# Optimization experiments

Hardware: AMD Instinct MI355X
Metric: run time of the kernel (lower is better)

The kernel has to match this reference:

```python
import jax, jax.numpy as jnp
import numpy as np

N = 100000       # num nodes
E = 1600000      # num edges
IN_DIM = 128
HID = 128
HEADS = 4
HEAD_DIM = HID // HEADS  # 32
NEG_SLOPE = 0.2
LN_EPS = 1e-5


def _glorot(key, shape):
    fan_in, fan_out = shape[-1], shape[0]
    limit = float(np.sqrt(6.0 / (fan_in + fan_out)))
    return jax.random.uniform(key, shape, jnp.float32, -limit, limit)


def setup_inputs() -> dict:
    key = jax.random.key(0)
    ks = jax.random.split(key, 16)
    return {
        "x": jax.random.normal(ks[0], (N, IN_DIM), jnp.float32),
        "edge_index": jax.random.randint(ks[1], (2, E), 0, N, jnp.int64),
        # embedding Linear(IN_DIM -> HID)
        "W_emb": _glorot(ks[2], (HID, IN_DIM)),
        "b_emb": jnp.zeros((HID,), jnp.float32),
        # E8 layer weight (F.linear, no bias)
        "W_e8": _glorot(ks[3], (HID, HID)),
        # GATConv: lin weight [HID, HEADS*HEAD_DIM], attention vectors, output bias
        "W_gat": _glorot(ks[4], (HEADS * HEAD_DIM, HID)),
        "att_src": _glorot(ks[5], (HEADS, HEAD_DIM)),
        "att_dst": _glorot(ks[6], (HEADS, HEAD_DIM)),
        "b_gat": jnp.zeros((HEADS * HEAD_DIM,), jnp.float32),
        # fusion Linear(2*HID -> HID)
        "W_fus": _glorot(ks[7], (HID, 2 * HID)),
        "b_fus": jnp.zeros((HID,), jnp.float32),
        # LayerNorm(HID)
        "gamma": jnp.ones((HID,), jnp.float32),
        "beta": jnp.zeros((HID,), jnp.float32),
        # readout MLP HID -> HID//2 -> 1
        "W_r1": _glorot(ks[8], (HID // 2, HID)),
        "b_r1": jnp.zeros((HID // 2,), jnp.float32),
        "W_r2": _glorot(ks[9], (1, HID // 2)),
        "b_r2": jnp.zeros((1,), jnp.float32),
    }


def reference(x, edge_index, W_emb, b_emb, W_e8, W_gat, att_src, att_dst,
              b_gat, W_fus, b_fus, gamma, beta, W_r1, b_r1, W_r2, b_r2):
    row = edge_index[0]  # src
    col = edge_index[1]  # dst

    # embedding
    h = x @ W_emb.T + b_emb          # [N, HID]
    res = h

    # --- E8: sparse normalized-adjacency matmul + linear ---
    deg = jax.ops.segment_sum(jnp.ones((E,), h.dtype), col, num_segments=N)
    dinv = jnp.where(deg > 0, deg ** -0.5, 0.0)
    vals = dinv[row] * dinv[col]                       # [E]
    agg = jax.ops.segment_sum(h[col] * vals[:, None], row, num_segments=N)
    x_e8 = agg @ W_e8.T                                # [N, HID]

    # --- GATConv (heads=4, concat, add_self_loops) ---
    loop = jnp.arange(N, dtype=row.dtype)
    src = jnp.concatenate([row, loop])                 # [E+N]
    dst = jnp.concatenate([col, loop])
    g = (h @ W_gat.T).reshape(N, HEADS, HEAD_DIM)      # [N, H, C]
    a_src = (g * att_src).sum(-1)                      # [N, H]
    a_dst = (g * att_dst).sum(-1)
    e = jax.nn.leaky_relu(a_src[src] + a_dst[dst], NEG_SLOPE)  # [E+N, H]
    m = jax.ops.segment_max(e, dst, num_segments=N)    # scatter-softmax max
    e = jnp.exp(e - m[dst])
    s = jax.ops.segment_sum(e, dst, num_segments=N)
    alpha = e / (s[dst] + 1e-16)                       # [E+N, H]
    msg = g[src] * alpha[..., None]                    # [E+N, H, C]
    x_gat = jax.ops.segment_sum(msg, dst, num_segments=N).reshape(N, HEADS * HEAD_DIM) + b_gat

    # --- fusion + residual + LayerNorm + ReLU ---
    f = jnp.concatenate([x_e8, x_gat], axis=-1) @ W_fus.T + b_fus
    z = f + res
    mu = z.mean(-1, keepdims=True)
    var = ((z - mu) ** 2).mean(-1, keepdims=True)
    z = (z - mu) * jax.lax.rsqrt(var + LN_EPS) * gamma + beta
    z = jax.nn.relu(z)  # dropout is identity in eval mode

    # --- readout MLP + sigmoid ---
    r = jax.nn.relu(z @ W_r1.T + b_r1)
    out = jax.nn.sigmoid(r @ W_r2.T + b_r2)            # [N, 1]
    return out
```

## Files before the change

kernel.cpp:

```cpp
#include <hip/hip_runtime.h>
#include <hip/hip_bf16.h>
#include <math.h>

#define NWIN 16
#define NCHUNK 128
#define CAP 64

typedef __attribute__((ext_vector_type(8))) short bf16x8;
typedef __attribute__((ext_vector_type(4))) float f32x4;
typedef __attribute__((ext_vector_type(2))) int i32x2;

__device__ __forceinline__ float us2f(unsigned short u) {
    return __uint_as_float(((unsigned)u) << 16);
}
__device__ __forceinline__ unsigned short f2bf(float f) {
    unsigned u = __float_as_uint(f);
    u += 0x7FFF + ((u >> 16) & 1);
    return (unsigned short)(u >> 16);
}

__global__ void setup_kernel(const float* __restrict__ b_gat, const float* __restrict__ W_fus,
                             const float* __restrict__ b_fus, float* __restrict__ bfus2,
                             const float* __restrict__ We, const float* __restrict__ W8,
                             const float* __restrict__ Wg, unsigned short* __restrict__ W16,
                             int* __restrict__ cnt, int total) {
    int b = blockIdx.x;
    if (b == 0) {
        int t = threadIdx.x;
        if (t < 128) {
            float acc = b_fus[t];
            for (int k = 0; k < 128; k++)
                acc += b_gat[k] * W_fus[t * 256 + 128 + k];
            bfus2[t] = acc;
        }
        return;
    }
    if (b <= 320) {
        int i = (b - 1) * 256 + threadIdx.x;
        if (i < 81920) {
            float v;
            if (i < 16384) v = We[i];
            else if (i < 32768) v = W8[i - 16384];
            else if (i < 49152) v = Wg[i - 32768];
            else v = W_fus[i - 49152];
            W16[i] = f2bf(v);
        }
        return;
    }
    int i = (b - 321) * 256 + threadIdx.x;
    if (i < total) cnt[i] = 0;
}

__global__ __launch_bounds__(256) void fill_win(
    const int* __restrict__ row, const int* __restrict__ col,
    int* __restrict__ cnt, int* __restrict__ adjF, int E, int N, int win) {
    int b = blockIdx.x;
    int w = (b & 7) | (((b >> 10) & 1) << 3);
    int chunk = (b >> 3) & (NCHUNK - 1);
    int lo = w * win, hi = lo + win;
    int per = (E + NCHUNK - 1) / NCHUNK;
    per = (per + 1) & ~1;
    int s = chunk * per;
    int e_end = s + per; if (e_end > E) e_end = E;

    for (int i = s + threadIdx.x * 2; i < e_end; i += 512) {
        int r0, r1, c0, c1;
        if (i + 1 < e_end) {
            i32x2 rv = __builtin_nontemporal_load((const i32x2*)(row + i));
            i32x2 cv = __builtin_nontemporal_load((const i32x2*)(col + i));
            r0 = rv[0]; r1 = rv[1]; c0 = cv[0]; c1 = cv[1];
        } else {
            r0 = row[i]; r1 = -1;
            c0 = col[i]; c1 = 0;
        }
        if (c0 >= lo && c0 < hi) {
            int p = atomicAdd(&cnt[c0], 1);
            if (p < CAP) adjF[(size_t)c0 * CAP + p] = r0;
        }
        int k2 = N + r0;
        if (k2 >= lo && k2 < hi) {
            int p = atomicAdd(&cnt[k2], 1);
            if (p < CAP) adjF[(size_t)k2 * CAP + p] = c0;
        }
        if (r1 >= 0) {
            if (c1 >= lo && c1 < hi) {
                int p = atomicAdd(&cnt[c1], 1);
                if (p < CAP) adjF[(size_t)c1 * CAP + p] = r1;
            }
            int k3 = N + r1;
            if (k3 >= lo && k3 < hi) {
                int p = atomicAdd(&cnt[k3], 1);
                if (p < CAP) adjF[(size_t)k3 * CAP + p] = c1;
            }
        }
    }
}

__global__ void dinv_kernel(const int* __restrict__ cnt, float* __restrict__ dinv, int N) {
    int i = blockIdx.x * 256 + threadIdx.x;
    if (i < N) {
        int d = cnt[i];
        dinv[i] = d > 0 ? rsqrtf((float)d) : 0.0f;
    }
}

template <bool A_FP32, bool HAS_BIAS, bool OUT_BF16, bool OUT_SC, bool OUT_ATT>
__global__ __launch_bounds__(256) void gemm_mfma(
    const void* __restrict__ A_, const unsigned short* __restrict__ W16,
    const float* __restrict__ bias, unsigned short* __restrict__ C16,
    const float* __restrict__ rsc, unsigned short* __restrict__ Csc,
    const float* __restrict__ attS, const float* __restrict__ attD,
    float* __restrict__ aS, float* __restrict__ aD, int n) {
    const int t = threadIdx.x;
    const int wave = t >> 6, lane = t & 63;
    const int quad = lane >> 4, ln = lane & 15;
    const int row0 = blockIdx.x * 128 + wave * 32;
    const int kq = quad * 8;

    f32x4 zero = {0.f, 0.f, 0.f, 0.f};
    f32x4 acc[2][8];
#pragma unroll
    for (int i = 0; i < 2; i++)
#pragma unroll
        for (int j = 0; j < 8; j++) acc[i][j] = zero;

#pragma unroll
    for (int ks = 0; ks < 4; ks++) {
        bf16x8 a[2];
#pragma unroll
        for (int mt = 0; mt < 2; mt++) {
            int row = row0 + mt * 16 + ln;
            if (row >= n) row = n - 1;
            if (A_FP32) {
                const float* ap = (const float*)A_ + (size_t)row * 128 + ks * 32 + kq;
                float4 f0 = *(const float4*)ap;
                float4 f1 = *(const float4*)(ap + 4);
                bf16x8 v;
                v[0] = (short)f2bf(f0.x); v[1] = (short)f2bf(f0.y);
                v[2] = (short)f2bf(f0.z); v[3] = (short)f2bf(f0.w);
                v[4] = (short)f2bf(f1.x); v[5] = (short)f2bf(f1.y);
                v[6] = (short)f2bf(f1.z); v[7] = (short)f2bf(f1.w);
                a[mt] = v;
            } else {
                a[mt] = *(const bf16x8*)((const unsigned short*)A_ +
                                         (size_t)row * 128 + ks * 32 + kq);
            }
        }
#pragma unroll
        for (int nt = 0; nt < 8; nt++) {
            bf16x8 b = *(const bf16x8*)(W16 + (size_t)(nt * 16 + ln) * 128 + ks * 32 + kq);
            acc[0][nt] = __builtin_amdgcn_mfma_f32_16x16x32_bf16(a[0], b, acc[0][nt], 0, 0, 0);
            acc[1][nt] = __builtin_amdgcn_mfma_f32_16x16x32_bf16(a[1], b, acc[1][nt], 0, 0, 0);
        }
    }

    float bv[8];
    if (HAS_BIAS) {
#pragma unroll
        for (int nt = 0; nt < 8; nt++) bv[nt] = bias[nt * 16 + ln];
    }
    float asv[8], adv[8];
    if (OUT_ATT) {
#pragma unroll
        for (int nt = 0; nt < 8; nt++) {
            int idx = (nt >> 1) * 32 + (nt & 1) * 16 + ln;
            asv[nt] = attS[idx];
            adv[nt] = attD[idx];
        }
    }
#pragma unroll
    for (int mt = 0; mt < 2; mt++) {
        int rbase = row0 + mt * 16 + quad * 4;
#pragma unroll
        for (int reg = 0; reg < 4; reg++) {
            int row = rbase + reg;
            if (row >= n) continue;
            float sc = OUT_SC ? rsc[row] : 0.f;
            if (OUT_ATT) {
                float ps[4] = {0.f, 0.f, 0.f, 0.f};
                float pd[4] = {0.f, 0.f, 0.f, 0.f};
#pragma unroll
                for (int nt = 0; nt < 8; nt++) {
                    float v = acc[mt][nt][reg];
                    ps[nt >> 1] += v * asv[nt];
                    pd[nt >> 1] += v * adv[nt];
                }
#pragma unroll
                for (int m = 1; m < 16; m <<= 1) {
#pragma unroll
                    for (int hh = 0; hh < 4; hh++) {
                        ps[hh] += __shfl_xor(ps[hh], m);
                        pd[hh] += __shfl_xor(pd[hh], m);
                    }
                }
                if (ln == 0) {
                    *(float4*)&aS[(size_t)row * 4] = make_float4(ps[0], ps[1], ps[2], ps[3]);
                    *(float4*)&aD[(size_t)row * 4] = make_float4(pd[0], pd[1], pd[2], pd[3]);
                }
            }
#pragma unroll
            for (int nt = 0; nt < 8; nt++) {
                float v = acc[mt][nt][reg];
                if (HAS_BIAS) v += bv[nt];
                int col = nt * 16 + ln;
                if (OUT_BF16) C16[(size_t)row * 128 + col] = f2bf(v);
                if (OUT_SC) Csc[(size_t)row * 128 + col] = f2bf(v * sc);
            }
        }
    }
}

__global__ __launch_bounds__(256) void fusion_ln_mfma(
    const unsigned short* __restrict__ xe816, const unsigned short* __restrict__ xg16,
    const unsigned short* __restrict__ Wf16,
    const float* __restrict__ bfus2, const unsigned short* __restrict__ h16,
    const float* __restrict__ gamma, const float* __restrict__ beta,
    unsigned short* __restrict__ z16, int n) {
    const int t = threadIdx.x;
    const int wave = t >> 6, lane = t & 63;
    const int quad = lane >> 4, ln = lane & 15;
    const int row0 = blockIdx.x * 128 + wave * 32;
    const int kq = quad * 8;

    f32x4 zero = {0.f, 0.f, 0.f, 0.f};
    f32x4 acc[2][8];
#pragma unroll
    for (int i = 0; i < 2; i++)
#pragma unroll
        for (int j = 0; j < 8; j++) acc[i][j] = zero;

    for (int half = 0; half < 2; half++) {
        const unsigned short* A = half ? xg16 : xe816;
#pragma unroll
        for (int ks = 0; ks < 4; ks++) {
            bf16x8 a[2];
#pragma unroll
            for (int mt = 0; mt < 2; mt++) {
                int row = row0 + mt * 16 + ln;
                if (row >= n) row = n - 1;
                a[mt] = *(const bf16x8*)(A + (size_t)row * 128 + ks * 32 + kq);
            }
#pragma unroll
            for (int nt = 0; nt < 8; nt++) {
                bf16x8 b = *(const bf16x8*)(Wf16 + (size_t)(nt * 16 + ln) * 256 +
                                            half * 128 + ks * 32 + kq);
                acc[0][nt] = __builtin_amdgcn_mfma_f32_16x16x32_bf16(a[0], b, acc[0][nt], 0, 0, 0);
                acc[1][nt] = __builtin_amdgcn_mfma_f32_16x16x32_bf16(a[1], b, acc[1][nt], 0, 0, 0);
            }
        }
    }

    float bv[8], gm[8], bt[8];
#pragma unroll
    for (int nt = 0; nt < 8; nt++) {
        int c = nt * 16 + ln;
        bv[nt] = bfus2[c]; gm[nt] = gamma[c]; bt[nt] = beta[c];
    }
#pragma unroll
    for (int mt = 0; mt < 2; mt++) {
#pragma unroll
        for (int reg = 0; reg < 4; reg++) {
            int row = row0 + mt * 16 + quad * 4 + reg;
            if (row >= n) continue;
            float v[8];
            float s1 = 0.f, s2 = 0.f;
#pragma unroll
            for (int nt = 0; nt < 8; nt++) {
                float x = acc[mt][nt][reg] + bv[nt] +
                          us2f(h16[(size_t)row * 128 + nt * 16 + ln]);
                v[nt] = x; s1 += x; s2 += x * x;
            }
#pragma unroll
            for (int m = 1; m < 16; m <<= 1) {
                s1 += __shfl_xor(s1, m);
                s2 += __shfl_xor(s2, m);
            }
            float mu = s1 * (1.f / 128.f);
            float var = s2 * (1.f / 128.f) - mu * mu;
            float inv = rsqrtf(var + 1e-5f);
#pragma unroll
            for (int nt = 0; nt < 8; nt++) {
                float o = (v[nt] - mu) * inv * gm[nt] + bt[nt];
                o = o > 0.f ? o : 0.f;
                z16[(size_t)row * 128 + nt * 16 + ln] = f2bf(o);
            }
        }
    }
}

__global__ __launch_bounds__(256) void e8_gather(
    const int* __restrict__ cnt, const int* __restrict__ adjF,
    const float* __restrict__ dinv, const unsigned short* __restrict__ hd16,
    unsigned short* __restrict__ agg16, int N) {
    int r = blockIdx.x * 4 + (threadIdx.x >> 6);
    int lane = threadIdx.x & 63;
    if (r >= N) return;
    int key = N + r;
    int m = min(cnt[key], CAP);
    int av = (lane < m) ? adjF[(size_t)key * CAP + lane] : 0;
    float ax = 0.f, ay = 0.f;
    int j = 0;
    for (; j + 8 <= m; j += 8) {
        int c[8]; ushort2 hv[8];
#pragma unroll
        for (int q = 0; q < 8; q++) c[q] = __shfl(av, j + q);
#pragma unroll
        for (int q = 0; q < 8; q++)
            hv[q] = *(const ushort2*)&hd16[(size_t)c[q] * 128 + lane * 2];
#pragma unroll
        for (int q = 0; q < 8; q++) { ax += us2f(hv[q].x); ay += us2f(hv[q].y); }
    }
    for (; j < m; j++) {
        int c = __shfl(av, j);
        ushort2 hv = *(const ushort2*)&hd16[(size_t)c * 128 + lane * 2];
        ax += us2f(hv.x);
        ay += us2f(hv.y);
    }
    float dr = dinv[r];
    ushort2 o; o.x = f2bf(ax * dr); o.y = f2bf(ay * dr);
    *(ushort2*)&agg16[(size_t)r * 128 + lane * 2] = o;
}

__global__ __launch_bounds__(256) void gat_gather(
    const int* __restrict__ cnt, const int* __restrict__ adjF,
    const float* __restrict__ a_src, const float* __restrict__ a_dst,
    const unsigned short* __restrict__ g16, unsigned short* __restrict__ xg16, int N) {
    int d = blockIdx.x * 4 + (threadIdx.x >> 6);
    int lane = threadIdx.x & 63;
    if (d >= N) return;
    int hd = lane >> 4;
    float ad = a_dst[d * 4 + hd];

    float e = a_src[d * 4 + hd] + ad; e = e > 0.f ? e : 0.2f * e;
    float m0 = e, l = 1.f;
    ushort2 gv0 = *(const ushort2*)&g16[(size_t)d * 128 + lane * 2];
    float accx = us2f(gv0.x), accy = us2f(gv0.y);

    int mm = min(cnt[d], CAP);
    int av = (lane < mm) ? adjF[(size_t)d * CAP + lane] : 0;
    int j = 0;
    for (; j + 4 <= mm; j += 4) {
        int s[4]; float tv[4]; ushort2 gu[4];
#pragma unroll
        for (int q = 0; q < 4; q++) s[q] = __shfl(av, j + q);
#pragma unroll
        for (int q = 0; q < 4; q++) tv[q] = a_src[s[q] * 4 + hd];
#pragma unroll
        for (int q = 0; q < 4; q++)
            gu[q] = *(const ushort2*)&g16[(size_t)s[q] * 128 + lane * 2];
        float mn = m0;
#pragma unroll
        for (int q = 0; q < 4; q++) {
            tv[q] += ad;
            tv[q] = tv[q] > 0.f ? tv[q] : 0.2f * tv[q];
            mn = fmaxf(mn, tv[q]);
        }
        float sc = __expf(m0 - mn);
        float wsum = 0.f, axp = 0.f, ayp = 0.f;
#pragma unroll
        for (int q = 0; q < 4; q++) {
            float wq = __expf(tv[q] - mn);
            wsum += wq;
            axp += wq * us2f(gu[q].x);
            ayp += wq * us2f(gu[q].y);
        }
        accx = accx * sc + axp;
        accy = accy * sc + ayp;
        l = l * sc + wsum;
        m0 = mn;
    }
    for (; j < mm; j++) {
        int s = __shfl(av, j);
        float t0 = a_src[s * 4 + hd] + ad; t0 = t0 > 0.f ? t0 : 0.2f * t0;
        ushort2 gu = *(const ushort2*)&g16[(size_t)s * 128 + lane * 2];
        float mn = fmaxf(m0, t0);
        float sc = __expf(m0 - mn), w = __expf(t0 - mn);
        accx = accx * sc + w * us2f(gu.x);
        accy = accy * sc + w * us2f(gu.y);
        l = l * sc + w;
        m0 = mn;
    }
    float inv = 1.f / l;
    ushort2 o; o.x = f2bf(accx * inv); o.y = f2bf(accy * inv);
    *(ushort2*)&xg16[(size_t)d * 128 + lane * 2] = o;
}

__global__ __launch_bounds__(256) void readout_kernel(
    const unsigned short* __restrict__ z16, const float* __restrict__ W1,
    const float* __restrict__ b1, const float* __restrict__ W2,
    const float* __restrict__ b2, float* __restrict__ out, int N) {
    __shared__ float zs[32 * 132];
    __shared__ float wlds[64 * 132];
    __shared__ float w2s[64];
    __shared__ float b1s[64];
    const int t = threadIdx.x;
    const int row0 = blockIdx.x * 32;

    for (int i = 0; i < 4; i++) {
        int idx = i * 256 + t;
        int r = idx >> 5, c4 = idx & 31;
        float4 v = make_float4(0.f, 0.f, 0.f, 0.f);
        if (row0 + r < N) {
            ushort4 u = *(const ushort4*)&z16[(size_t)(row0 + r) * 128 + c4 * 4];
            v = make_float4(us2f(u.x), us2f(u.y), us2f(u.z), us2f(u.w));
        }
        *(float4*)&zs[r * 132 + c4 * 4] = v;
    }
    for (int i = 0; i < 8; i++) {
        int idx = i * 256 + t;
        int o = idx >> 5, c4 = idx & 31;
        *(float4*)&wlds[o * 132 + c4 * 4] = *(const float4*)&W1[o * 128 + c4 * 4];
    }
    if (t < 64) { w2s[t] = W2[t]; b1s[t] = b1[t]; }
    __syncthreads();

    const int rg = t >> 4;
    const int cg = t & 15;
    float acc[2][4] = {};
    const float* z0 = &zs[(rg * 2) * 132];
    const float* z1 = z0 + 132;
    for (int k4 = 0; k4 < 32; k4++) {
        float4 a0 = *(const float4*)&z0[k4 * 4];
        float4 a1 = *(const float4*)&z1[k4 * 4];
#pragma unroll
        for (int j = 0; j < 4; j++) {
            float4 wv = *(const float4*)&wlds[(cg * 4 + j) * 132 + k4 * 4];
            acc[0][j] += a0.x * wv.x + a0.y * wv.y + a0.z * wv.z + a0.w * wv.w;
            acc[1][j] += a1.x * wv.x + a1.y * wv.y + a1.z * wv.z + a1.w * wv.w;
        }
    }
    float p0 = 0.f, p1 = 0.f;
#pragma unroll
    for (int j = 0; j < 4; j++) {
        int o = cg * 4 + j;
        float r0 = acc[0][j] + b1s[o]; r0 = r0 > 0.f ? r0 : 0.f;
        float r1 = acc[1][j] + b1s[o]; r1 = r1 > 0.f ? r1 : 0.f;
        p0 += r0 * w2s[o]; p1 += r1 * w2s[o];
    }
    for (int off = 8; off > 0; off >>= 1) {
        p0 += __shfl_down(p0, off, 16);
        p1 += __shfl_down(p1, off, 16);
    }
    if (cg == 0) {
        float bb = b2[0];
        int r0i = row0 + rg * 2, r1i = r0i + 1;
        if (r0i < N) out[r0i] = 1.f / (1.f + __expf(-(p0 + bb)));
        if (r1i < N) out[r1i] = 1.f / (1.f + __expf(-(p1 + bb)));
    }
}

extern "C" void kernel_launch(void* const* d_in, const int* in_sizes, int n_in,
                              void* d_out, int out_size, void* d_ws, size_t ws_size,
                              hipStream_t stream) {
    const float* x     = (const float*)d_in[0];
    const int*   ei    = (const int*)d_in[1];
    const float* W_emb = (const float*)d_in[2];
    const float* b_emb = (const float*)d_in[3];
    const float* W_e8  = (const float*)d_in[4];
    const float* W_gat = (const float*)d_in[5];
    const float* att_s = (const float*)d_in[6];
    const float* att_d = (const float*)d_in[7];
    const float* b_gat = (const float*)d_in[8];
    const float* W_fus = (const float*)d_in[9];
    const float* b_fus = (const float*)d_in[10];
    const float* gamma = (const float*)d_in[11];
    const float* beta  = (const float*)d_in[12];
    const float* W_r1  = (const float*)d_in[13];
    const float* b_r1  = (const float*)d_in[14];
    const float* W_r2  = (const float*)d_in[15];
    const float* b_r2  = (const float*)d_in[16];

    const int N = in_sizes[0] / 128;
    const int E = in_sizes[1] / 2;
    const int* rowp = ei;
    const int* colp = ei + E;
    const int total = 2 * N;
    const int win = (total + NWIN - 1) / NWIN;
    const int GB = (N + 127) / 128;

    const size_t NF = (size_t)N * 128;
    char* base = (char*)d_ws;
    unsigned short* h16   = (unsigned short*)base;
    unsigned short* hd16  = h16 + NF;
    unsigned short* bufA  = hd16 + NF;
    unsigned short* xe816 = bufA + NF;
    unsigned short* g16   = xe816 + NF;
    int*            adjF  = (int*)(g16 + NF);
    unsigned short* z16   = (unsigned short*)adjF;
    float* dinv  = (float*)(adjF + NF);
    float* a_src = dinv + N;
    float* a_dst = a_src + (size_t)4 * N;
    float* bfus2 = a_dst + (size_t)4 * N;
    unsigned short* W16a = (unsigned short*)(bfus2 + 128);
    unsigned short* We16 = W16a;
    unsigned short* W816 = W16a + 16384;
    unsigned short* Wg16 = W16a + 32768;
    unsigned short* Wf16 = W16a + 49152;
    int* cnt = (int*)(W16a + 81920);

    int setup_grid = 321 + (total + 255) / 256;
    setup_kernel<<<setup_grid, 256, 0, stream>>>(b_gat, W_fus, b_fus, bfus2,
                                                 W_emb, W_e8, W_gat, W16a, cnt, total);
    fill_win<<<2048, 256, 0, stream>>>(rowp, colp, cnt, adjF, E, N, win);
    dinv_kernel<<<(N + 255) / 256, 256, 0, stream>>>(cnt, dinv, N);

    gemm_mfma<true, true, true, true, false><<<GB, 256, 0, stream>>>(
        x, We16, b_emb, h16, dinv, hd16, nullptr, nullptr, nullptr, nullptr, N);

    e8_gather<<<(N + 3) / 4, 256, 0, stream>>>(cnt, adjF, dinv, hd16, bufA, N);
    gemm_mfma<false, false, true, false, false><<<GB, 256, 0, stream>>>(
        bufA, W816, nullptr, xe816, nullptr, nullptr, nullptr, nullptr,
        nullptr, nullptr, N);

    gemm_mfma<false, false, true, false, true><<<GB, 256, 0, stream>>>(
        h16, Wg16, nullptr, g16, nullptr, nullptr, att_s, att_d, a_src, a_dst, N);
    gat_gather<<<(N + 3) / 4, 256, 0, stream>>>(cnt, adjF, a_src, a_dst, g16, bufA, N);

    fusion_ln_mfma<<<GB, 256, 0, stream>>>(xe816, bufA, Wf16, bfus2, h16,
                                           gamma, beta, z16, N);

    readout_kernel<<<(N + 31) / 32, 256, 0, stream>>>(z16, W_r1, b_r1, W_r2, b_r2,
                                                      (float*)d_out, N);
}
```

Baseline: 625.8 us.

## Co-schedule independent GEMM and gather stages in combined kernel launches

Independent stages now share a launch by splitting the grid on block index. The embedding GEMM runs alongside the adjacency fill, the GAT projection GEMM alongside the E8 gather, and the E8 weight GEMM alongside the GAT softmax gather. This cuts the launch count and lets compute-bound GEMM blocks overlap with memory-bound gather blocks. Other changes: E8 now reads dinv per neighbor instead of a prescaled copy of h, the GAT softmax computes the max in one wave-wide pass instead of an online rescale, and the fill window/chunk counts and nontemporal loads are changed. Costs include an extra dinv read per edge and register pressure from mixing kernel bodies in one launch.

Measured after the change: 789.2 us. 1.26x slower.

```diff
diff --git a/kernel.cpp b/kernel.cpp
--- a/kernel.cpp
+++ b/kernel.cpp
@@ -2,13 +2,12 @@
 #include <hip/hip_bf16.h>
 #include <math.h>
 
-#define NWIN 16
-#define NCHUNK 128
+#define NWIN 8
+#define NCHUNK 256
 #define CAP 64
 
 typedef __attribute__((ext_vector_type(8))) short bf16x8;
 typedef __attribute__((ext_vector_type(4))) float f32x4;
-typedef __attribute__((ext_vector_type(2))) int i32x2;
 
 __device__ __forceinline__ float us2f(unsigned short u) {
     return __uint_as_float(((unsigned)u) << 16);
@@ -51,70 +50,59 @@
     if (i < total) cnt[i] = 0;
 }
 
-__global__ __launch_bounds__(256) void fill_win(
-    const int* __restrict__ row, const int* __restrict__ col,
+__device__ __forceinline__ void fill_body(
+    int bid, const int* __restrict__ row, const int* __restrict__ col,
     int* __restrict__ cnt, int* __restrict__ adjF, int E, int N, int win) {
-    int b = blockIdx.x;
-    int w = (b & 7) | (((b >> 10) & 1) << 3);
-    int chunk = (b >> 3) & (NCHUNK - 1);
+    int w = bid & (NWIN - 1);
+    int chunk = bid >> 3;
     int lo = w * win, hi = lo + win;
     int per = (E + NCHUNK - 1) / NCHUNK;
     per = (per + 1) & ~1;
     int s = chunk * per;
     int e_end = s + per; if (e_end > E) e_end = E;
 
-    for (int i = s + threadIdx.x * 2; i < e_end; i += 512) {
-        int r0, r1, c0, c1;
+    for (int i = s + (int)threadIdx.x * 2; i < e_end; i += 512) {
+        int2 rv, cv;
         if (i + 1 < e_end) {
-            i32x2 rv = __builtin_nontemporal_load((const i32x2*)(row + i));
-            i32x2 cv = __builtin_nontemporal_load((const i32x2*)(col + i));
-            r0 = rv[0]; r1 = rv[1]; c0 = cv[0]; c1 = cv[1];
+            rv = *(const int2*)(row + i);
+            cv = *(const int2*)(col + i);
         } else {
-            r0 = row[i]; r1 = -1;
-            c0 = col[i]; c1 = 0;
-        }
-        if (c0 >= lo && c0 < hi) {
-            int p = atomicAdd(&cnt[c0], 1);
-            if (p < CAP) adjF[(size_t)c0 * CAP + p] = r0;
-        }
-        int k2 = N + r0;
+            rv.x = row[i]; rv.y = -1;
+            cv.x = col[i]; cv.y = 0;
+        }
+        if (cv.x >= lo && cv.x < hi) {
+            int p = atomicAdd(&cnt[cv.x], 1);
+            if (p < CAP) adjF[(size_t)cv.x * CAP + p] = rv.x;
+        }
+        int k2 = N + rv.x;
         if (k2 >= lo && k2 < hi) {
             int p = atomicAdd(&cnt[k2], 1);
-            if (p < CAP) adjF[(size_t)k2 * CAP + p] = c0;
-        }
-        if (r1 >= 0) {
-            if (c1 >= lo && c1 < hi) {
-                int p = atomicAdd(&cnt[c1], 1);
-                if (p < CAP) adjF[(size_t)c1 * CAP + p] = r1;
-            }
-            int k3 = N + r1;
+            if (p < CAP) adjF[(size_t)k2 * CAP + p] = cv.x;
+        }
+        if (rv.y >= 0) {
+            if (cv.y >= lo && cv.y < hi) {
+                int p = atomicAdd(&cnt[cv.y], 1);
+                if (p < CAP) adjF[(size_t)cv.y * CAP + p] = rv.y;
+            }
+            int k3 = N + rv.y;
             if (k3 >= lo && k3 < hi) {
                 int p = atomicAdd(&cnt[k3], 1);
-                if (p < CAP) adjF[(size_t)k3 * CAP + p] = c1;
-            }
-        }
-    }
-}
-
-__global__ void dinv_kernel(const int* __restrict__ cnt, float* __restrict__ dinv, int N) {
-    int i = blockIdx.x * 256 + threadIdx.x;
-    if (i < N) {
-        int d = cnt[i];
-        dinv[i] = d > 0 ? rsqrtf((float)d) : 0.0f;
-    }
-}
-
-template <bool A_FP32, bool HAS_BIAS, bool OUT_BF16, bool OUT_SC, bool OUT_ATT>
-__global__ __launch_bounds__(256) void gemm_mfma(
-    const void* __restrict__ A_, const unsigned short* __restrict__ W16,
+                if (p < CAP) adjF[(size_t)k3 * CAP + p] = cv.y;
+            }
+        }
+    }
+}
+
+template <bool A_FP32, bool HAS_BIAS, bool OUT_ATT>
+__device__ __forceinline__ void gemm_body(
+    int bid, const void* __restrict__ A_, const unsigned short* __restrict__ W16,
     const float* __restrict__ bias, unsigned short* __restrict__ C16,
-    const float* __restrict__ rsc, unsigned short* __restrict__ Csc,
     const float* __restrict__ attS, const float* __restrict__ attD,
     float* __restrict__ aS, float* __restrict__ aD, int n) {
     const int t = threadIdx.x;
     const int wave = t >> 6, lane = t & 63;
     const int quad = lane >> 4, ln = lane & 15;
-    const int row0 = blockIdx.x * 128 + wave * 32;
+    const int row0 = bid * 128 + wave * 32;
     const int kq = quad * 8;
 
     f32x4 zero = {0.f, 0.f, 0.f, 0.f};
@@ -175,7 +163,6 @@
         for (int reg = 0; reg < 4; reg++) {
             int row = rbase + reg;
             if (row >= n) continue;
-            float sc = OUT_SC ? rsc[row] : 0.f;
             if (OUT_ATT) {
                 float ps[4] = {0.f, 0.f, 0.f, 0.f};
                 float pd[4] = {0.f, 0.f, 0.f, 0.f};
@@ -202,11 +189,195 @@
             for (int nt = 0; nt < 8; nt++) {
                 float v = acc[mt][nt][reg];
                 if (HAS_BIAS) v += bv[nt];
-                int col = nt * 16 + ln;
-                if (OUT_BF16) C16[(size_t)row * 128 + col] = f2bf(v);
-                if (OUT_SC) Csc[(size_t)row * 128 + col] = f2bf(v * sc);
-            }
-        }
+                C16[(size_t)row * 128 + nt * 16 + ln] = f2bf(v);
+            }
+        }
+    }
+}
+
+__device__ __forceinline__ void e8_body(
+    int bid, const int* __restrict__ cnt, const int* __restrict__ adjF,
+    const float* __restrict__ dinv, const unsigned short* __restrict__ h16,
+    unsigned short* __restrict__ agg16, int N) {
+    int r = bid * 4 + ((int)threadIdx.x >> 6);
+    int lane = threadIdx.x & 63;
+    if (r >= N) return;
+    int key = N + r;
+    int m = min(cnt[key], CAP);
+    int av = (lane < m) ? adjF[(size_t)key * CAP + lane] : 0;
+    float ax = 0.f, ay = 0.f;
+    int j = 0;
+    for (; j + 8 <= m; j += 8) {
+        int c[8]; float dv[8]; ushort2 hv[8];
+#pragma unroll
+        for (int q = 0; q < 8; q++) c[q] = __shfl(av, j + q);
+#pragma unroll
+        for (int q = 0; q < 8; q++) dv[q] = dinv[c[q]];
+#pragma unroll
+        for (int q = 0; q < 8; q++)
+            hv[q] = *(const ushort2*)&h16[(size_t)c[q] * 128 + lane * 2];
+#pragma unroll
+        for (int q = 0; q < 8; q++) {
+            ax += us2f(hv[q].x) * dv[q];
+            ay += us2f(hv[q].y) * dv[q];
+        }
+    }
+    for (; j < m; j++) {
+        int c = __shfl(av, j);
+        float dv = dinv[c];
+        ushort2 hv = *(const ushort2*)&h16[(size_t)c * 128 + lane * 2];
+        ax += us2f(hv.x) * dv;
+        ay += us2f(hv.y) * dv;
+    }
+    float dr = dinv[r];
+    ushort2 o; o.x = f2bf(ax * dr); o.y = f2bf(ay * dr);
+    *(ushort2*)&agg16[(size_t)r * 128 + lane * 2] = o;
+}
+
+__device__ __forceinline__ void gat_body(
+    int bid, const int* __restrict__ cnt, const int* __restrict__ adjF,
+    const float* __restrict__ a_src, const float* __restrict__ a_dst,
+    const unsigned short* __restrict__ g16, unsigned short* __restrict__ xg16,
+    int N, float* __restrict__ wlds) {
+    int d = bid * 4 + ((int)threadIdx.x >> 6);
+    int lane = threadIdx.x & 63;
+    int wave = threadIdx.x >> 6;
+    if (d >= N) return;
+    float* wl = wlds + wave * 272;
+
+    float4 ad4 = *(const float4*)&a_dst[(size_t)d * 4];
+    float4 asd = *(const float4*)&a_src[(size_t)d * 4];
+    float adh[4] = {ad4.x, ad4.y, ad4.z, ad4.w};
+    float tS[4] = {asd.x + ad4.x, asd.y + ad4.y, asd.z + ad4.z, asd.w + ad4.w};
+#pragma unroll
+    for (int h = 0; h < 4; h++) tS[h] = tS[h] > 0.f ? tS[h] : 0.2f * tS[h];
+
+    int mm = min(cnt[d], CAP);
+    int av = (lane < mm) ? adjF[(size_t)d * CAP + lane] : 0;
+
+    float t[4];
+    if (lane < mm) {
+        float4 a4 = *(const float4*)&a_src[(size_t)av * 4];
+        float ta[4] = {a4.x, a4.y, a4.z, a4.w};
+#pragma unroll
+        for (int h = 0; h < 4; h++) {
+            float e = ta[h] + adh[h];
+            t[h] = e > 0.f ? e : 0.2f * e;
+        }
+    } else {
+#pragma unroll
+        for (int h = 0; h < 4; h++) t[h] = -3e38f;
+    }
+    float m[4];
+#pragma unroll
+    for (int h = 0; h < 4; h++) m[h] = t[h];
+#pragma unroll
+    for (int off = 1; off < 64; off <<= 1) {
+#pragma unroll
+        for (int h = 0; h < 4; h++) m[h] = fmaxf(m[h], __shfl_xor(m[h], off));
+    }
+#pragma unroll
+    for (int h = 0; h < 4; h++) m[h] = fmaxf(m[h], tS[h]);
+
+    float w_[4], l[4];
+#pragma unroll
+    for (int h = 0; h < 4; h++) {
+        w_[h] = (lane < mm) ? __expf(t[h] - m[h]) : 0.f;
+        l[h] = w_[h];
+    }
+#pragma unroll
+    for (int off = 1; off < 64; off <<= 1) {
+#pragma unroll
+        for (int h = 0; h < 4; h++) l[h] += __shfl_xor(l[h], off);
+    }
+    float wS[4];
+#pragma unroll
+    for (int h = 0; h < 4; h++) {
+        wS[h] = __expf(tS[h] - m[h]);
+        l[h] += wS[h];
+        wl[h * 68 + lane] = w_[h];
+    }
+
+    int hd = lane >> 4;
+    ushort2 g0 = *(const ushort2*)&g16[(size_t)d * 128 + lane * 2];
+    float accx = wS[hd] * us2f(g0.x), accy = wS[hd] * us2f(g0.y);
+    const float* wh = wl + hd * 68;
+    int j = 0;
+    for (; j + 4 <= mm; j += 4) {
+        int s[4]; float wv[4]; ushort2 gu[4];
+#pragma unroll
+        for (int q = 0; q < 4; q++) s[q] = __shfl(av, j + q);
+#pragma unroll
+        for (int q = 0; q < 4; q++) wv[q] = wh[j + q];
+#pragma unroll
+        for (int q = 0; q < 4; q++)
+            gu[q] = *(const ushort2*)&g16[(size_t)s[q] * 128 + lane * 2];
+#pragma unroll
+        for (int q = 0; q < 4; q++) {
+            accx += wv[q] * us2f(gu[q].x);
+            accy += wv[q] * us2f(gu[q].y);
+        }
+    }
+    for (; j < mm; j++) {
+        int s = __shfl(av, j);
+        float wv = wh[j];
+        ushort2 gu = *(const ushort2*)&g16[(size_t)s * 128 + lane * 2];
+        accx += wv * us2f(gu.x);
+        accy += wv * us2f(gu.y);
+    }
+    float inv = 1.f / l[hd];
+    ushort2 o; o.x = f2bf(accx * inv); o.y = f2bf(accy * inv);
+    *(ushort2*)&xg16[(size_t)d * 128 + lane * 2] = o;
+}
+
+
+__global__ __launch_bounds__(256) void fill_emb_kernel(
+    const float* __restrict__ x, const unsigned short* __restrict__ We16,
+    const float* __restrict__ b_emb, unsigned short* __restrict__ h16,
+    const int* __restrict__ row, const int* __restrict__ col,
+    int* __restrict__ cnt, int* __restrict__ adjF, int E, int N, int win, int GB) {
+    int b = blockIdx.x;
+    if (b < GB)
+        gemm_body<true, true, false>(b, x, We16, b_emb, h16,
+                                     nullptr, nullptr, nullptr, nullptr, N);
+    else
+        fill_body(b - GB, row, col, cnt, adjF, E, N, win);
+}
+
+__global__ __launch_bounds__(256) void g_e8_kernel(
+    const unsigned short* __restrict__ h16, const unsigned short* __restrict__ Wg16,
+    unsigned short* __restrict__ g16, const float* __restrict__ attS,
+    const float* __restrict__ attD, float* __restrict__ aS, float* __restrict__ aD,
+    const int* __restrict__ cnt, const int* __restrict__ adjF,
+    const float* __restrict__ dinv, unsigned short* __restrict__ agg16,
+    int N, int GB) {
+    int b = blockIdx.x;
+    if (b < GB)
+        gemm_body<false, false, true>(b, h16, Wg16, nullptr, g16, attS, attD, aS, aD, N);
+    else
+        e8_body(b - GB, cnt, adjF, dinv, h16, agg16, N);
+}
+
+__global__ __launch_bounds__(256) void e8g_gat_kernel(
+    const unsigned short* __restrict__ agg16, const unsigned short* __restrict__ W816,
+    unsigned short* __restrict__ xe816, const int* __restrict__ cnt,
+    const int* __restrict__ adjF, const float* __restrict__ a_src,
+    const float* __restrict__ a_dst, const unsigned short* __restrict__ g16,
+    unsigned short* __restrict__ xg16, int N, int GB) {
+    __shared__ float wlds[4 * 272];
+    int b = blockIdx.x;
+    if (b < GB)
+        gemm_body<false, false, false>(b, agg16, W816, nullptr, xe816,
+                                       nullptr, nullptr, nullptr, nullptr, N);
+    else
+        gat_body(b - GB, cnt, adjF, a_src, a_dst, g16, xg16, N, wlds);
+}
+
+__global__ void dinv_kernel(const int* __restrict__ cnt, float* __restrict__ dinv, int N) {
+    int i = blockIdx.x * 256 + threadIdx.x;
+    if (i < N) {
+        int d = cnt[i];
+        dinv[i] = d > 0 ? rsqrtf((float)d) : 0.0f;
     }
 }
 
@@ -286,103 +457,6 @@
             }
         }
     }
-}
-
-__global__ __launch_bounds__(256) void e8_gather(
-    const int* __restrict__ cnt, const int* __restrict__ adjF,
-    const float* __restrict__ dinv, const unsigned short* __restrict__ hd16,
-    unsigned short* __restrict__ agg16, int N) {
-    int r = blockIdx.x * 4 + (threadIdx.x >> 6);
-    int lane = threadIdx.x & 63;
-    if (r >= N) return;
-    int key = N + r;
-    int m = min(cnt[key], CAP);
-    int av = (lane < m) ? adjF[(size_t)key * CAP + lane] : 0;
-    float ax = 0.f, ay = 0.f;
-    int j = 0;
-    for (; j + 8 <= m; j += 8) {
-        int c[8]; ushort2 hv[8];
-#pragma unroll
-        for (int q = 0; q < 8; q++) c[q] = __shfl(av, j + q);
-#pragma unroll
-        for (int q = 0; q < 8; q++)
-            hv[q] = *(const ushort2*)&hd16[(size_t)c[q] * 128 + lane * 2];
-#pragma unroll
-        for (int q = 0; q < 8; q++) { ax += us2f(hv[q].x); ay += us2f(hv[q].y); }
-    }
-    for (; j < m; j++) {
-        int c = __shfl(av, j);
-        ushort2 hv = *(const ushort2*)&hd16[(size_t)c * 128 + lane * 2];
-        ax += us2f(hv.x);
-        ay += us2f(hv.y);
-    }
-    float dr = dinv[r];
-    ushort2 o; o.x = f2bf(ax * dr); o.y = f2bf(ay * dr);
-    *(ushort2*)&agg16[(size_t)r * 128 + lane * 2] = o;
-}
-
-__global__ __launch_bounds__(256) void gat_gather(
-    const int* __restrict__ cnt, const int* __restrict__ adjF,
-    const float* __restrict__ a_src, const float* __restrict__ a_dst,
-    const unsigned short* __restrict__ g16, unsigned short* __restrict__ xg16, int N) {
-    int d = blockIdx.x * 4 + (threadIdx.x >> 6);
-    int lane = threadIdx.x & 63;
-    if (d >= N) return;
-    int hd = lane >> 4;
-    float ad = a_dst[d * 4 + hd];
-
-    float e = a_src[d * 4 + hd] + ad; e = e > 0.f ? e : 0.2f * e;
-    float m0 = e, l = 1.f;
-    ushort2 gv0 = *(const ushort2*)&g16[(size_t)d * 128 + lane * 2];
-    float accx = us2f(gv0.x), accy = us2f(gv0.y);
-
-    int mm = min(cnt[d], CAP);
-    int av = (lane < mm) ? adjF[(size_t)d * CAP + lane] : 0;
-    int j = 0;
-    for (; j + 4 <= mm; j += 4) {
-        int s[4]; float tv[4]; ushort2 gu[4];
-#pragma unroll
-        for (int q = 0; q < 4; q++) s[q] = __shfl(av, j + q);
-#pragma unroll
-        for (int q = 0; q < 4; q++) tv[q] = a_src[s[q] * 4 + hd];
-#pragma unroll
-        for (int q = 0; q < 4; q++)
-            gu[q] = *(const ushort2*)&g16[(size_t)s[q] * 128 + lane * 2];
-        float mn = m0;
-#pragma unroll
-        for (int q = 0; q < 4; q++) {
-            tv[q] += ad;
-            tv[q] = tv[q] > 0.f ? tv[q] : 0.2f * tv[q];
-            mn = fmaxf(mn, tv[q]);
-        }
-        float sc = __expf(m0 - mn);
-        float wsum = 0.f, axp = 0.f, ayp = 0.f;
-#pragma unroll
-        for (int q = 0; q < 4; q++) {
-            float wq = __expf(tv[q] - mn);
-            wsum += wq;
-            axp += wq * us2f(gu[q].x);
-            ayp += wq * us2f(gu[q].y);
-        }
-        accx = accx * sc + axp;
-        accy = accy * sc + ayp;
-        l = l * sc + wsum;
-        m0 = mn;
-    }
-    for (; j < mm; j++) {
-        int s = __shfl(av, j);
-        float t0 = a_src[s * 4 + hd] + ad; t0 = t0 > 0.f ? t0 : 0.2f * t0;
-        ushort2 gu = *(const ushort2*)&g16[(size_t)s * 128 + lane * 2];
-        float mn = fmaxf(m0, t0);
-        float sc = __expf(m0 - mn), w = __expf(t0 - mn);
-        accx = accx * sc + w * us2f(gu.x);
-        accy = accy * sc + w * us2f(gu.y);
-        l = l * sc + w;
-        m0 = mn;
-    }
-    float inv = 1.f / l;
-    ushort2 o; o.x = f2bf(accx * inv); o.y = f2bf(accy * inv);
-    *(ushort2*)&xg16[(size_t)d * 128 + lane * 2] = o;
 }
 
 __global__ __launch_bounds__(256) void readout_kernel(
@@ -477,15 +551,16 @@
     const int total = 2 * N;
     const int win = (total + NWIN - 1) / NWIN;
     const int GB = (N + 127) / 128;
+    const int GATB = (N + 3) / 4;
 
     const size_t NF = (size_t)N * 128;
     char* base = (char*)d_ws;
     unsigned short* h16   = (unsigned short*)base;
-    unsigned short* hd16  = h16 + NF;
-    unsigned short* bufA  = hd16 + NF;
+    unsigned short* bufA  = h16 + NF;
     unsigned short* xe816 = bufA + NF;
     unsigned short* g16   = xe816 + NF;
-    int*            adjF  = (int*)(g16 + NF);
+    unsigned short* xg16  = g16 + NF;
+    int*            adjF  = (int*)(xg16 + NF);
     unsigned short* z16   = (unsigned short*)adjF;
     float* dinv  = (float*)(adjF + NF);
     float* a_src = dinv + N;
@@ -501,22 +576,19 @@
     int setup_grid = 321 + (total + 255) / 256;
     setup_kernel<<<setup_grid, 256, 0, stream>>>(b_gat, W_fus, b_fus, bfus2,
                                                  W_emb, W_e8, W_gat, W16a, cnt, total);
-    fill_win<<<2048, 256, 0, stream>>>(rowp, colp, cnt, adjF, E, N, win);
+
+    fill_emb_kernel<<<GB + NWIN * NCHUNK, 256, 0, stream>>>(
+        x, We16, b_emb, h16, rowp, colp, cnt, adjF, E, N, win, GB);
+
     dinv_kernel<<<(N + 255) / 256, 256, 0, stream>>>(cnt, dinv, N);
 
-    gemm_mfma<true, true, true, true, false><<<GB, 256, 0, stream>>>(
-        x, We16, b_emb, h16, dinv, hd16, nullptr, nullptr, nullptr, nullptr, N);
-
-    e8_gather<<<(N + 3) / 4, 256, 0, stream>>>(cnt, adjF, dinv, hd16, bufA, N);
-    gemm_mfma<false, false, true, false, false><<<GB, 256, 0, stream>>>(
-        bufA, W816, nullptr, xe816, nullptr, nullptr, nullptr, nullptr,
-        nullptr, nullptr, N);
-
-    gemm_mfma<false, false, true, false, true><<<GB, 256, 0, stream>>>(
-        h16, Wg16, nullptr, g16, nullptr, nullptr, att_s, att_d, a_src, a_dst, N);
-    gat_gather<<<(N + 3) / 4, 256, 0, stream>>>(cnt, adjF, a_src, a_dst, g16, bufA, N);
-
-    fusion_ln_mfma<<<GB, 256, 0, stream>>>(xe816, bufA, Wf16, bfus2, h16,
+    g_e8_kernel<<<GB + GATB, 256, 0, stream>>>(
+        h16, Wg16, g16, att_s, att_d, a_src, a_dst, cnt, adjF, dinv, bufA, N, GB);
+
+    e8g_gat_kernel<<<GB + GATB, 256, 0, stream>>>(
+        bufA, W816, xe816, cnt, adjF, a_src, a_dst, g16, xg16, N, GB);
+
+    fusion_ln_mfma<<<GB, 256, 0, stream>>>(xe816, xg16, Wf16, bfus2, h16,
                                            gamma, beta, z16, N);
 
     readout_kernel<<<(N + 31) / 32, 256, 0, stream>>>(z16, W_r1, b_r1, W_r2, b_r2,
```
